# Performance work log

Measured on AMD Instinct MI355X. Metric: run time of the kernel, lower is better.

The kernel has to match this reference:

```python
import jax, jax.numpy as jnp
import numpy as np

EPSILON = 1e-8

def setup_inputs() -> dict:
    key = jax.random.key(0)
    k1, k2, k3, k4 = jax.random.split(key, 4)
    B, C_in, C_out, H, W, S, K = 16, 512, 512, 32, 32, 512, 3
    x = jax.random.normal(k1, (B, C_in, H, W), dtype=jnp.float32)
    w = jax.random.normal(k2, (B, S), dtype=jnp.float32)
    # Linear(style_dim -> in_chan), bias initialized to ones per module code
    style_w = jax.random.normal(k3, (C_in, S), dtype=jnp.float32) * (1.0 / np.sqrt(S))
    style_b = jnp.ones((C_in,), dtype=jnp.float32)
    # kaiming_normal_(fan_in, leaky_relu): std = sqrt(2/(1+0.01^2)) / sqrt(fan_in)
    fan_in = C_in * K * K
    gain = np.sqrt(2.0 / (1.0 + 0.01 ** 2))
    weight = jax.random.normal(k4, (C_out, C_in, K, K), dtype=jnp.float32) * (gain / np.sqrt(fan_in))
    return {"x": x, "w": w, "style_w": style_w, "style_b": style_b, "weight": weight}

def reference(x, w, style_w, style_b, weight):
    B, C, H, W_ = x.shape
    C_out, _, K, _ = weight.shape
    # style modulation: Linear(style_dim -> in_chan)
    style = w @ style_w.T + style_b                       # (B, C_in)
    weights = style[:, None, :, None, None] * weight[None]  # (B, C_out, C_in, K, K)
    # demodulation
    d = jax.lax.rsqrt(jnp.sum(weights * weights, axis=(2, 3, 4), keepdims=True) + EPSILON)
    weights = weights * d
    # grouped conv with groups = batch
    pad = 1 if K > 1 else 0
    xg = x.reshape(1, B * C, H, W_)
    wg = weights.reshape(B * C_out, C, K, K)
    y = jax.lax.conv_general_dilated(
        xg, wg, window_strides=(1, 1), padding=((pad, pad), (pad, pad)),
        dimension_numbers=("NCHW", "OIHW", "NCHW"), feature_group_count=B)
    return y.reshape(B, C_out, H, W_)
```

## Files before the change

kernel.cpp:

```cpp
#include <hip/hip_runtime.h>
#include <hip/hip_bf16.h>

#define NB 16
#define CI 512
#define CO 512
#define HW 1024
#define SD 512
#define EPSI 1e-8f

typedef __attribute__((ext_vector_type(8))) short bf16x8;
typedef __attribute__((ext_vector_type(16))) float f32x16;
typedef __attribute__((ext_vector_type(4))) unsigned int u32x4;

#define GLOAD_LDS16(g, l) __builtin_amdgcn_global_load_lds( \
    (const __attribute__((address_space(1))) unsigned int*)(const void*)(g), \
    (__attribute__((address_space(3))) unsigned int*)(void*)(l), 16, 0, 0)

__global__ void k_style2(const float* __restrict__ w, const float* __restrict__ sw,
                         const float* __restrict__ sb, float* __restrict__ style) {
    int gw = (blockIdx.x * 256 + threadIdx.x) >> 6;
    int l = threadIdx.x & 63;
    int b = gw >> 9, c = gw & 511;
    const float4* wr = (const float4*)(w + b * SD) + (l << 1);
    const float4* sr = (const float4*)(sw + c * SD) + (l << 1);
    float4 a0 = wr[0], a1 = wr[1], q0 = sr[0], q1 = sr[1];
    float acc = a0.x * q0.x + a0.y * q0.y + a0.z * q0.z + a0.w * q0.w
              + a1.x * q1.x + a1.y * q1.y + a1.z * q1.z + a1.w * q1.w;
#pragma unroll
    for (int off = 32; off > 0; off >>= 1) acc += __shfl_down(acc, off);
    if (l == 0) style[gw] = acc + sb[c];
}

__global__ void k_wprep(const float* __restrict__ wt, float* __restrict__ wsq,
                        __hip_bfloat16* __restrict__ wtb) {
    int idx = blockIdx.x * 256 + threadIdx.x;
    const float* p = wt + idx * 9;
    float a = 0.f;
#pragma unroll
    for (int t = 0; t < 9; ++t) {
        float v = p[t];
        a += v * v;
        wtb[t * (CO * CI) + idx] = __float2bfloat16(v);
    }
    wsq[idx] = a;
}

__global__ void k_demod2(const float* __restrict__ style, const float* __restrict__ wsq,
                         float* __restrict__ dv) {
    int gw = (blockIdx.x * 256 + threadIdx.x) >> 6;
    int l = threadIdx.x & 63;
    int b = gw >> 9, co = gw & 511;
    const float4* st = (const float4*)(style + b * CI) + (l << 1);
    const float4* wq = (const float4*)(wsq + co * CI) + (l << 1);
    float4 s0 = st[0], s1 = st[1], q0 = wq[0], q1 = wq[1];
    float acc = s0.x * s0.x * q0.x + s0.y * s0.y * q0.y + s0.z * s0.z * q0.z + s0.w * s0.w * q0.w
              + s1.x * s1.x * q1.x + s1.y * s1.y * q1.y + s1.z * s1.z * q1.z + s1.w * s1.w * q1.w;
#pragma unroll
    for (int off = 32; off > 0; off >>= 1) acc += __shfl_down(acc, off);
    if (l == 0) dv[gw] = rsqrtf(acc + EPSI);
}

__global__ void k_xs(const float* __restrict__ x, const float* __restrict__ style,
                     __hip_bfloat16* __restrict__ xs) {
    __shared__ float tile[32][33];
    int b = blockIdx.z, c0 = blockIdx.y * 32, p0 = blockIdx.x * 32;
    int tx = threadIdx.x & 31, ty = threadIdx.x >> 5;
#pragma unroll
    for (int i = 0; i < 4; ++i) {
        int ci = c0 + ty + i * 8;
        tile[ty + i * 8][tx] = x[(b * CI + ci) * HW + p0 + tx] * style[b * CI + ci];
    }
    __syncthreads();
#pragma unroll
    for (int i = 0; i < 4; ++i) {
        int p = p0 + ty + i * 8;
        xs[(b * HW + p) * CI + c0 + tx] = __float2bfloat16(tile[tx][ty + i * 8]);
    }
}

#define XS_BYTES 52224
#define WBUF_BYTES 16384

extern "C" __global__ __launch_bounds__(256, 1) void k_conv(
        const __hip_bfloat16* __restrict__ wtb,
        const __hip_bfloat16* __restrict__ xs,
        const float* __restrict__ dvec,
        float* __restrict__ out) {
    extern __shared__ char smem[];
    char* Xs  = smem;
    char* Wsb = smem + XS_BYTES;

    const int tid  = threadIdx.x;
    const int lane = tid & 63;
    const int wv   = tid >> 6;
    const int wn   = wv & 1;
    const int wb   = wv >> 1;

    int bid = blockIdx.x;
    int xcd = bid & 7, idx = bid >> 3;
    int cot = xcd >> 1;
    int px8 = idx & 7;
    int bp  = (idx >> 3) | ((xcd & 1) << 2);
    const int co0 = cot * 128;
    const int p0  = px8 * 128;
    const int y0  = px8 * 4;
    const int b0  = bp * 2;
    const int b   = b0 + wb;

    if (tid < 192) {
        int g = tid & 7;
        int rx = ((tid >> 3) & 1) ? 33 : 0;
        int row = tid >> 4;
        *(u32x4*)(Xs + (row * 34 + rx) * 128 + g * 16) = (u32x4){0, 0, 0, 0};
    }

    f32x16 acc[4][2];
#pragma unroll
    for (int m = 0; m < 4; ++m)
#pragma unroll
        for (int n = 0; n < 2; ++n)
            acc[m][n] = (f32x16)(0.f);

    {
        const __hip_bfloat16* wsrc = wtb + (size_t)co0 * CI;
        int srcg = (lane & 7) ^ (lane >> 3);
#pragma unroll
        for (int k = 0; k < 4; ++k) {
            int seg = k * 4 + wv;
            int co_l = seg * 8 + (lane >> 3);
            GLOAD_LDS16(wsrc + co_l * CI + srcg * 8, Wsb + seg * 1024);
        }
    }

    for (int cc = 0; cc < 8; ++cc) {
        const int ci0 = cc * 64;
        if (cc) __syncthreads();
#pragma unroll
        for (int k = 0; k < 12; ++k) {
            int sid = k * 4 + wv;
            int bb = (k >= 6) ? 1 : 0;
            int rem = sid - bb * 24;
            int ry = rem >> 2, seg = rem & 3;
            int rx0 = 1 + seg * 8;
            char* ldst = Xs + ((bb * 6 + ry) * 34 + rx0) * 128;
            int y = y0 - 1 + ry;
            int rx = rx0 + (lane >> 3);
            int srcg = (lane & 7) ^ (rx & 7);
            if ((unsigned)y < 32u) {
                GLOAD_LDS16(xs + ((size_t)(b0 + bb) * HW + (y << 5) + (rx - 1)) * CI + ci0 + srcg * 8,
                            ldst);
            } else {
                *(u32x4*)(ldst + (lane << 4)) = (u32x4){0, 0, 0, 0};
            }
        }

#pragma unroll
        for (int t = 0; t < 9; ++t) {
            __syncthreads();
            if (cc * 9 + t < 71) {
                const int tn = (t == 8) ? 0 : (t + 1);
                const int cin = (t == 8) ? (ci0 + 64) : ci0;
                const __hip_bfloat16* wsrc = wtb + ((size_t)tn * CO + co0) * CI + cin;
                char* wdst = Wsb + (((cc + t + 1) & 1) ? WBUF_BYTES : 0);
                int srcg = (lane & 7) ^ (lane >> 3);
#pragma unroll
                for (int k = 0; k < 4; ++k) {
                    int seg = k * 4 + wv;
                    int co_l = seg * 8 + (lane >> 3);
                    GLOAD_LDS16(wsrc + co_l * CI + srcg * 8, wdst + seg * 1024);
                }
            }
            const char* Wb = Wsb + (((cc + t) & 1) ? WBUF_BYTES : 0);
            const int ky = t / 3, kx = t - (t / 3) * 3;
#pragma unroll
            for (int q = 0; q < 4; ++q) {
                bf16x8 afr[4], bfr[2];
                int g = (q << 1) + (lane >> 5);
#pragma unroll
                for (int m = 0; m < 4; ++m)
                    afr[m] = *(const bf16x8*)(Wb + (m * 32 + (lane & 31)) * 128 +
                                              ((g ^ (lane & 7)) << 4));
#pragma unroll
                for (int n = 0; n < 2; ++n) {
                    int ry = wn * 2 + n + ky;
                    int rx = (lane & 31) + kx;
                    bfr[n] = *(const bf16x8*)(Xs + ((wb * 6 + ry) * 34 + rx) * 128 +
                                              ((g ^ (rx & 7)) << 4));
                }
#pragma unroll
                for (int m = 0; m < 4; ++m)
#pragma unroll
                    for (int n = 0; n < 2; ++n)
                        acc[m][n] = __builtin_amdgcn_mfma_f32_32x32x16_bf16(afr[m], bfr[n], acc[m][n], 0, 0, 0);
            }
        }
    }

#pragma unroll
    for (int m = 0; m < 4; ++m) {
#pragma unroll
        for (int r = 0; r < 16; ++r) {
            int co = co0 + m * 32 + (r & 3) + ((r >> 2) << 3) + ((lane >> 5) << 2);
            float dvv = dvec[b * CO + co];
            float* orow = out + ((size_t)b * CO + co) * HW + p0 + wn * 64;
            orow[lane & 31]      = acc[m][0][r] * dvv;
            orow[32 + (lane & 31)] = acc[m][1][r] * dvv;
        }
    }
}

extern "C" void kernel_launch(void* const* d_in, const int* in_sizes, int n_in,
                              void* d_out, int out_size, void* d_ws, size_t ws_size,
                              hipStream_t stream) {
    const float* x  = (const float*)d_in[0];
    const float* w  = (const float*)d_in[1];
    const float* sw = (const float*)d_in[2];
    const float* sb = (const float*)d_in[3];
    const float* wt = (const float*)d_in[4];
    float* out = (float*)d_out;

    char* ws = (char*)d_ws;
    float* style = (float*)(ws);
    float* dvec  = (float*)(ws + 32768);
    float* wsq   = (float*)(ws + 65536);
    __hip_bfloat16* wtb = (__hip_bfloat16*)(ws + 1114112);
    __hip_bfloat16* xsb = (__hip_bfloat16*)(ws + 5832704);

    hipFuncSetAttribute((const void*)k_conv,
                        hipFuncAttributeMaxDynamicSharedMemorySize, 84992);

    k_style2<<<2048, 256, 0, stream>>>(w, sw, sb, style);
    k_wprep<<<1024, 256, 0, stream>>>(wt, wsq, wtb);
    k_xs<<<dim3(32, 16, 16), 256, 0, stream>>>(x, style, xsb);
    k_demod2<<<2048, 256, 0, stream>>>(style, wsq, dvec);
    k_conv<<<256, 256, 84992, stream>>>(wtb, xsb, dvec, out);
}
```

Measured before the change: 100.6 us.

## Double-buffer input tile and triple-buffer weights with explicit waitcnt pipelining in conv

The conv kernel now double-buffers the activation tile in LDS and prefetches the next channel chunk while computing the current one. This removes the stall that used to sit at the start of each chunk. Weight tiles move from double to triple buffering, issued two taps ahead. The __syncthreads calls are replaced by hand-tuned s_waitcnt vmcnt counts and raw s_barrier with sched barriers. LDS use grows to about 150KB. The hardcoded vmcnt values are fragile: if they are wrong, the kernel can produce incorrect results.

New measurement: 97.69 us. 1.03x faster.

```diff
diff --git a/kernel.cpp b/kernel.cpp
--- a/kernel.cpp
+++ b/kernel.cpp
@@ -15,6 +15,8 @@
 #define GLOAD_LDS16(g, l) __builtin_amdgcn_global_load_lds( \
     (const __attribute__((address_space(1))) unsigned int*)(const void*)(g), \
     (__attribute__((address_space(3))) unsigned int*)(void*)(l), 16, 0, 0)
+#define SCHED0() __builtin_amdgcn_sched_barrier(0)
+#define SBAR()   __builtin_amdgcn_s_barrier()
 
 __global__ void k_style2(const float* __restrict__ w, const float* __restrict__ sw,
                          const float* __restrict__ sb, float* __restrict__ style) {
@@ -80,6 +82,7 @@
 
 #define XS_BYTES 52224
 #define WBUF_BYTES 16384
+#define SMEM_TOTAL (2 * XS_BYTES + 3 * WBUF_BYTES)
 
 extern "C" __global__ __launch_bounds__(256, 1) void k_conv(
         const __hip_bfloat16* __restrict__ wtb,
@@ -88,7 +91,7 @@
         float* __restrict__ out) {
     extern __shared__ char smem[];
     char* Xs  = smem;
-    char* Wsb = smem + XS_BYTES;
+    char* Wsb = smem + 2 * XS_BYTES;
 
     const int tid  = threadIdx.x;
     const int lane = tid & 63;
@@ -106,35 +109,42 @@
     const int y0  = px8 * 4;
     const int b0  = bp * 2;
     const int b   = b0 + wb;
+    const bool xedge = (px8 == 0) || (px8 == 7);
 
     if (tid < 192) {
         int g = tid & 7;
         int rx = ((tid >> 3) & 1) ? 33 : 0;
         int row = tid >> 4;
-        *(u32x4*)(Xs + (row * 34 + rx) * 128 + g * 16) = (u32x4){0, 0, 0, 0};
-    }
-
-    f32x16 acc[4][2];
-#pragma unroll
-    for (int m = 0; m < 4; ++m)
-#pragma unroll
-        for (int n = 0; n < 2; ++n)
-            acc[m][n] = (f32x16)(0.f);
-
-    {
-        const __hip_bfloat16* wsrc = wtb + (size_t)co0 * CI;
-        int srcg = (lane & 7) ^ (lane >> 3);
+        int off = (row * 34 + rx) * 128 + g * 16;
+        *(u32x4*)(Xs + off) = (u32x4){0, 0, 0, 0};
+        *(u32x4*)(Xs + XS_BYTES + off) = (u32x4){0, 0, 0, 0};
+    }
+
+    const int srcgW = (lane & 7) ^ (lane >> 3);
+
+    auto issueW = [&](int tap, int cin, int bufi) {
+        const __hip_bfloat16* wsrc = wtb + ((size_t)tap * CO + co0) * CI + cin;
+        char* wdst = Wsb + bufi * WBUF_BYTES;
 #pragma unroll
         for (int k = 0; k < 4; ++k) {
             int seg = k * 4 + wv;
             int co_l = seg * 8 + (lane >> 3);
-            GLOAD_LDS16(wsrc + co_l * CI + srcg * 8, Wsb + seg * 1024);
-        }
-    }
-
-    for (int cc = 0; cc < 8; ++cc) {
-        const int ci0 = cc * 64;
-        if (cc) __syncthreads();
+            GLOAD_LDS16(wsrc + co_l * CI + srcgW * 8, wdst + seg * 1024);
+        }
+    };
+    auto issueX = (void*)nullptr; (void)issueX;
+
+    f32x16 acc[4][2];
+#pragma unroll
+    for (int m = 0; m < 4; ++m)
+#pragma unroll
+        for (int n = 0; n < 2; ++n)
+            acc[m][n] = (f32x16)(0.f);
+
+    issueW(0, 0, 0);
+    issueW(1, 0, 1);
+    {
+        char* Xdst = Xs;
 #pragma unroll
         for (int k = 0; k < 12; ++k) {
             int sid = k * 4 + wv;
@@ -142,35 +152,54 @@
             int rem = sid - bb * 24;
             int ry = rem >> 2, seg = rem & 3;
             int rx0 = 1 + seg * 8;
-            char* ldst = Xs + ((bb * 6 + ry) * 34 + rx0) * 128;
+            char* ldst = Xdst + ((bb * 6 + ry) * 34 + rx0) * 128;
             int y = y0 - 1 + ry;
             int rx = rx0 + (lane >> 3);
             int srcg = (lane & 7) ^ (rx & 7);
-            if ((unsigned)y < 32u) {
-                GLOAD_LDS16(xs + ((size_t)(b0 + bb) * HW + (y << 5) + (rx - 1)) * CI + ci0 + srcg * 8,
-                            ldst);
-            } else {
+            if ((unsigned)y < 32u)
+                GLOAD_LDS16(xs + ((size_t)(b0 + bb) * HW + (y << 5) + (rx - 1)) * CI + 0 + srcg * 8, ldst);
+            else
                 *(u32x4*)(ldst + (lane << 4)) = (u32x4){0, 0, 0, 0};
-            }
-        }
-
+        }
+    }
+    SCHED0();
+    asm volatile("s_waitcnt lgkmcnt(0) vmcnt(0)" ::: "memory");
+    SCHED0();
+    SBAR();
+    SCHED0();
+
+    for (int cc = 0; cc < 8; ++cc) {
+        const char* Xcur = Xs + (cc & 1) * XS_BYTES;
 #pragma unroll
         for (int t = 0; t < 9; ++t) {
-            __syncthreads();
-            if (cc * 9 + t < 71) {
-                const int tn = (t == 8) ? 0 : (t + 1);
-                const int cin = (t == 8) ? (ci0 + 64) : ci0;
-                const __hip_bfloat16* wsrc = wtb + ((size_t)tn * CO + co0) * CI + cin;
-                char* wdst = Wsb + (((cc + t + 1) & 1) ? WBUF_BYTES : 0);
-                int srcg = (lane & 7) ^ (lane >> 3);
-#pragma unroll
-                for (int k = 0; k < 4; ++k) {
-                    int seg = k * 4 + wv;
-                    int co_l = seg * 8 + (lane >> 3);
-                    GLOAD_LDS16(wsrc + co_l * CI + srcg * 8, wdst + seg * 1024);
+            if (!(cc == 7 && t >= 7)) {
+                const int tn  = (t <= 6) ? (t + 2) : (t - 7);
+                const int cin = ((t <= 6) ? cc : (cc + 1)) * 64;
+                issueW(tn, cin, (t + 2) % 3);
+            }
+            if (t == 0 && cc < 7) {
+                char* Xdst = Xs + ((cc + 1) & 1) * XS_BYTES;
+                const int cin = (cc + 1) * 64;
+#pragma unroll
+                for (int k = 0; k < 12; ++k) {
+                    int sid = k * 4 + wv;
+                    int bb = (k >= 6) ? 1 : 0;
+                    int rem = sid - bb * 24;
+                    int ry = rem >> 2, seg = rem & 3;
+                    int rx0 = 1 + seg * 8;
+                    char* ldst = Xdst + ((bb * 6 + ry) * 34 + rx0) * 128;
+                    int y = y0 - 1 + ry;
+                    int rx = rx0 + (lane >> 3);
+                    int srcg = (lane & 7) ^ (rx & 7);
+                    if ((unsigned)y < 32u)
+                        GLOAD_LDS16(xs + ((size_t)(b0 + bb) * HW + (y << 5) + (rx - 1)) * CI + cin + srcg * 8, ldst);
+                    else
+                        *(u32x4*)(ldst + (lane << 4)) = (u32x4){0, 0, 0, 0};
                 }
             }
-            const char* Wb = Wsb + (((cc + t) & 1) ? WBUF_BYTES : 0);
+            SCHED0();
+
+            const char* Wb = Wsb + (t % 3) * WBUF_BYTES;
             const int ky = t / 3, kx = t - (t / 3) * 3;
 #pragma unroll
             for (int q = 0; q < 4; ++q) {
@@ -184,7 +213,7 @@
                 for (int n = 0; n < 2; ++n) {
                     int ry = wn * 2 + n + ky;
                     int rx = (lane & 31) + kx;
-                    bfr[n] = *(const bf16x8*)(Xs + ((wb * 6 + ry) * 34 + rx) * 128 +
+                    bfr[n] = *(const bf16x8*)(Xcur + ((wb * 6 + ry) * 34 + rx) * 128 +
                                               ((g ^ (rx & 7)) << 4));
                 }
 #pragma unroll
@@ -192,6 +221,21 @@
 #pragma unroll
                     for (int n = 0; n < 2; ++n)
                         acc[m][n] = __builtin_amdgcn_mfma_f32_32x32x16_bf16(afr[m], bfr[n], acc[m][n], 0, 0, 0);
+            }
+
+            if (!(cc == 7 && t == 8)) {
+                SCHED0();
+                if (cc < 7 && t < 2) {
+                    if (xedge) asm volatile("s_waitcnt lgkmcnt(0) vmcnt(14)" ::: "memory");
+                    else       asm volatile("s_waitcnt lgkmcnt(0) vmcnt(16)" ::: "memory");
+                } else if (cc == 7 && t == 7) {
+                    asm volatile("s_waitcnt lgkmcnt(0) vmcnt(0)" ::: "memory");
+                } else {
+                    asm volatile("s_waitcnt lgkmcnt(0) vmcnt(4)" ::: "memory");
+                }
+                SCHED0();
+                SBAR();
+                SCHED0();
             }
         }
     }
@@ -203,7 +247,7 @@
             int co = co0 + m * 32 + (r & 3) + ((r >> 2) << 3) + ((lane >> 5) << 2);
             float dvv = dvec[b * CO + co];
             float* orow = out + ((size_t)b * CO + co) * HW + p0 + wn * 64;
-            orow[lane & 31]      = acc[m][0][r] * dvv;
+            orow[lane & 31]        = acc[m][0][r] * dvv;
             orow[32 + (lane & 31)] = acc[m][1][r] * dvv;
         }
     }
@@ -227,11 +271,11 @@
     __hip_bfloat16* xsb = (__hip_bfloat16*)(ws + 5832704);
 
     hipFuncSetAttribute((const void*)k_conv,
-                        hipFuncAttributeMaxDynamicSharedMemorySize, 84992);
+                        hipFuncAttributeMaxDynamicSharedMemorySize, SMEM_TOTAL);
 
     k_style2<<<2048, 256, 0, stream>>>(w, sw, sb, style);
     k_wprep<<<1024, 256, 0, stream>>>(wt, wsq, wtb);
     k_xs<<<dim3(32, 16, 16), 256, 0, stream>>>(x, style, xsb);
     k_demod2<<<2048, 256, 0, stream>>>(style, wsq, dvec);
-    k_conv<<<256, 256, 84992, stream>>>(wtb, xsb, dvec, out);
-}
+    k_conv<<<256, 256, SMEM_TOTAL, stream>>>(wtb, xsb, dvec, out);
+}
```
